# Kernel tuning notes

Hardware: AMD Instinct MI355X
Metric: run time of the kernel (lower is better)

The kernel has to match this reference:

```python
import jax, jax.numpy as jnp
import numpy as np

B, T, S, C, E, H = 4, 2048, 2048, 256, 512, 8
D = E // H
SCALE = E ** (-0.5)


def setup_inputs() -> dict:
    key = jax.random.key(0)
    ks = jax.random.split(key, 12)
    x = jax.random.normal(ks[0], (B, T, C), dtype=jnp.float32)
    context = jax.random.normal(ks[1], (B, S, E), dtype=jnp.float32)
    pad_mask = jax.random.randint(ks[2], (B, T, S), 0, 2) == 1
    p = 0.02
    # Conv1d kernel_size=1 weights stored squeezed: [out_ch, in_ch]
    w_in = jax.random.normal(ks[3], (E, C), dtype=jnp.float32) * p
    b_in = jnp.zeros((E,), dtype=jnp.float32)
    wq = jax.random.normal(ks[4], (E, E), dtype=jnp.float32) * p
    bq = jnp.zeros((E,), dtype=jnp.float32)
    wk = jax.random.normal(ks[5], (E, E), dtype=jnp.float32) * p
    bk = jnp.zeros((E,), dtype=jnp.float32)
    wv = jax.random.normal(ks[6], (E, E), dtype=jnp.float32) * p
    bv = jnp.zeros((E,), dtype=jnp.float32)
    w_out = jax.random.normal(ks[7], (C, E), dtype=jnp.float32) * p
    b_out = jnp.zeros((C,), dtype=jnp.float32)
    return {"x": x, "context": context, "pad_mask": pad_mask,
            "w_in": w_in, "b_in": b_in, "wq": wq, "bq": bq,
            "wk": wk, "bk": bk, "wv": wv, "bv": bv,
            "w_out": w_out, "b_out": b_out}


def reference(x, context, pad_mask, w_in, b_in, wq, bq, wk, bk, wv, bv, w_out, b_out):
    # proj_in: Conv1d k=1 == per-token linear on channel dim. [B,T,C] -> [B,T,E]
    xe = jnp.einsum('btc,ec->bte', x, w_in) + b_in
    Q = (xe @ wq.T + bq).reshape(B, T, H, D)       # query tokens
    K = (context @ wk.T + bk).reshape(B, S, H, D)  # key tokens
    V = (context @ wv.T + bv).reshape(B, S, H, D)
    att = jnp.einsum('bihd,bjhd->bhij', Q, K) * SCALE  # [B,H,T,S]
    att = jnp.where(pad_mask[:, None, :, :], jnp.float32(-1e9), att)
    att = jax.nn.softmax(att, axis=-1)
    out = jnp.einsum('bhij,bjhd->bihd', att, V).reshape(B, T, E)
    # proj_out: Conv1d k=1, [B,T,E] -> [B,T,C]
    out = jnp.einsum('bte,ce->btc', out, w_out) + b_out
    return out
```

## Files before the change

### kernel.cpp

```cpp
#include <hip/hip_runtime.h>
#include <cstdint>
#include <cstddef>

#define Bb 4
#define Tt 2048
#define Ssz 2048
#define Cc 256
#define Ee 512
#define Hh 8

typedef short bf8 __attribute__((ext_vector_type(8)));
typedef float f4 __attribute__((ext_vector_type(4)));

__device__ __forceinline__ unsigned short f2bf(float x) {
  unsigned int u = __float_as_uint(x);
  u += 0x7fffu + ((u >> 16) & 1u);
  return (unsigned short)(u >> 16);
}

__device__ __forceinline__ bf8 cvt8(float4 a, float4 b) {
  bf8 r;
  r[0] = (short)f2bf(a.x); r[1] = (short)f2bf(a.y);
  r[2] = (short)f2bf(a.z); r[3] = (short)f2bf(a.w);
  r[4] = (short)f2bf(b.x); r[5] = (short)f2bf(b.y);
  r[6] = (short)f2bf(b.z); r[7] = (short)f2bf(b.w);
  return r;
}

__global__ __launch_bounds__(256) void prep(const float* __restrict__ w_in,
                                            const float* __restrict__ b_in,
                                            const float* __restrict__ wq,
                                            const float* __restrict__ bq,
                                            const float* __restrict__ wk,
                                            const float* __restrict__ wv,
                                            const float* __restrict__ wo,
                                            unsigned short* __restrict__ wkvb,
                                            unsigned short* __restrict__ wob,
                                            unsigned short* __restrict__ wqin,
                                            float* __restrict__ bqinb, float qsc) {
  __shared__ unsigned short sh[128][72];
  const int bid = blockIdx.x, tid = threadIdx.x;
  if (bid < 512) {
    int i = bid * 256 + tid;
    const float* s = (i < 65536) ? wk : wv;
    int off = (i < 65536) ? i : i - 65536;
    float4 v = ((const float4*)s)[off];
    ushort4 o;
    o.x = f2bf(v.x); o.y = f2bf(v.y); o.z = f2bf(v.z); o.w = f2bf(v.w);
    ((ushort4*)wkvb)[i] = o;
  } else if (bid < 640) {
    int i = (bid - 512) * 256 + tid;
    float4 v = ((const float4*)wo)[i];
    ushort4 o;
    o.x = f2bf(v.x); o.y = f2bf(v.y); o.z = f2bf(v.z); o.w = f2bf(v.w);
    ((ushort4*)wob)[i] = o;
  } else if (bid < 672) {
    const int idx = bid - 640;
    const int m0 = (idx & 7) * 64, n0 = (idx >> 3) * 64;
    unsigned short (*As)[72] = (unsigned short (*)[72]) & sh[0][0];
    unsigned short (*Bs)[72] = (unsigned short (*)[72]) & sh[64][0];
    const int wave = tid >> 6, lane = tid & 63;
    const int lrow = lane & 15, quad = lane >> 4;
    const int wm = (wave >> 1) * 32, wn = (wave & 1) * 32;
    const int arow = tid >> 3, ac = tid & 7;
    f4 acc[2][2];
#pragma unroll
    for (int i = 0; i < 2; i++)
#pragma unroll
      for (int j = 0; j < 2; j++) {
        f4 z = {0.f, 0.f, 0.f, 0.f};
        acc[i][j] = z;
      }
    for (int kt = 0; kt < 8; kt++) {
#pragma unroll
      for (int i = 0; i < 2; i++) {
        int row = arow + i * 32;
        const float* src = wq + (size_t)(m0 + row) * Ee + kt * 64 + ac * 8;
        float4 v0 = *(const float4*)src, v1 = *(const float4*)(src + 4);
        bf8 av;
        av[0] = (short)f2bf(v0.x * qsc); av[1] = (short)f2bf(v0.y * qsc);
        av[2] = (short)f2bf(v0.z * qsc); av[3] = (short)f2bf(v0.w * qsc);
        av[4] = (short)f2bf(v1.x * qsc); av[5] = (short)f2bf(v1.y * qsc);
        av[6] = (short)f2bf(v1.z * qsc); av[7] = (short)f2bf(v1.w * qsc);
        *(bf8*)&As[row][ac * 8] = av;
        int c = n0 + row;
        bf8 bv;
#pragma unroll
        for (int k = 0; k < 8; k++)
          bv[k] = (short)f2bf(w_in[(size_t)(kt * 64 + ac * 8 + k) * Cc + c]);
        *(bf8*)&Bs[row][ac * 8] = bv;
      }
      __syncthreads();
#pragma unroll
      for (int kk = 0; kk < 2; kk++) {
        bf8 af[2], bff[2];
#pragma unroll
        for (int i = 0; i < 2; i++) af[i] = *(const bf8*)&As[wm + i * 16 + lrow][kk * 32 + quad * 8];
#pragma unroll
        for (int j = 0; j < 2; j++) bff[j] = *(const bf8*)&Bs[wn + j * 16 + lrow][kk * 32 + quad * 8];
#pragma unroll
        for (int i = 0; i < 2; i++)
#pragma unroll
          for (int j = 0; j < 2; j++)
            acc[i][j] = __builtin_amdgcn_mfma_f32_16x16x32_bf16(af[i], bff[j], acc[i][j], 0, 0, 0);
      }
      __syncthreads();
    }
#pragma unroll
    for (int j = 0; j < 2; j++)
#pragma unroll
      for (int i = 0; i < 2; i++)
#pragma unroll
        for (int r = 0; r < 4; r++)
          wqin[(size_t)(m0 + wm + i * 16 + quad * 4 + r) * Cc + n0 + wn + j * 16 + lrow] =
              f2bf(acc[i][j][r]);
  } else {
    const int o = (bid - 672) * 32 + (tid >> 3);
    const int k0 = (tid & 7) * 64;
    float s = 0.f;
#pragma unroll
    for (int i = 0; i < 16; i++) {
      float4 w = *(const float4*)(wq + (size_t)o * Ee + k0 + i * 4);
      float4 bb = *(const float4*)(b_in + k0 + i * 4);
      s += w.x * bb.x + w.y * bb.y + w.z * bb.z + w.w * bb.w;
    }
    s += __shfl_xor(s, 1);
    s += __shfl_xor(s, 2);
    s += __shfl_xor(s, 4);
    if ((tid & 7) == 0) bqinb[o] = (s + bq[o]) * qsc;
  }
}

__global__ __launch_bounds__(256) void qkv(const float* __restrict__ x,
                                           const float* __restrict__ ctx,
                                           const unsigned short* __restrict__ wqin,
                                           const float* __restrict__ bqinb,
                                           const unsigned short* __restrict__ wkv,
                                           const float* __restrict__ bk,
                                           const float* __restrict__ bv,
                                           unsigned short* __restrict__ Qb,
                                           unsigned short* __restrict__ Kb,
                                           unsigned short* __restrict__ Vt,
                                           const int* __restrict__ mask,
                                           unsigned int* __restrict__ mp) {
  __shared__ unsigned short As[128][72];
  __shared__ unsigned short Bs[128][72];
  const int bid = blockIdx.x, tid = threadIdx.x;
  if (bid >= 768) {
    int i = (bid - 768) * 256 + tid;
    const int4* src = (const int4*)mask + (size_t)i * 8;
    unsigned int w = 0;
#pragma unroll
    for (int k = 0; k < 8; k++) {
      int4 v = src[k];
      w |= (unsigned int)(v.x != 0) << (k * 4);
      w |= (unsigned int)(v.y != 0) << (k * 4 + 1);
      w |= (unsigned int)(v.z != 0) << (k * 4 + 2);
      w |= (unsigned int)(v.w != 0) << (k * 4 + 3);
    }
    mp[i] = w;
    return;
  }
  const bool isQ = bid < 256;
  const int idx = isQ ? bid : bid - 256;
  const int m0 = (idx & 63) * 128;
  const int n0 = (idx >> 6) * 128;
  const int K = isQ ? 256 : 512;
  const float* A = isQ ? x : ctx;
  const unsigned short* Bt = isQ ? wqin : wkv;

  const int wave = tid >> 6, lane = tid & 63;
  const int lrow = lane & 15, quad = lane >> 4;
  const int wm = (wave >> 1) * 64, wn = (wave & 1) * 64;
  const int arow = tid >> 3, ac = tid & 7;

  f4 acc[4][4];
#pragma unroll
  for (int i = 0; i < 4; i++)
#pragma unroll
    for (int j = 0; j < 4; j++) {
      f4 z = {0.f, 0.f, 0.f, 0.f};
      acc[i][j] = z;
    }

  float4 ap0[4], ap1[4];
  bf8 bpre[4];
#pragma unroll
  for (int i = 0; i < 4; i++) {
    const float* src = A + (size_t)(m0 + arow + i * 32) * K + ac * 8;
    ap0[i] = *(const float4*)src;
    ap1[i] = *(const float4*)(src + 4);
    bpre[i] = *(const bf8*)(Bt + (size_t)(n0 + arow + i * 32) * K + ac * 8);
  }

  const int nkt = K >> 6;
  for (int kt = 0; kt < nkt; ++kt) {
#pragma unroll
    for (int i = 0; i < 4; i++) {
      *(bf8*)&As[arow + i * 32][ac * 8] = cvt8(ap0[i], ap1[i]);
      *(bf8*)&Bs[arow + i * 32][ac * 8] = bpre[i];
    }
    __syncthreads();
    if (kt + 1 < nkt) {
      int k0 = (kt + 1) << 6;
#pragma unroll
      for (int i = 0; i < 4; i++) {
        const float* src = A + (size_t)(m0 + arow + i * 32) * K + k0 + ac * 8;
        ap0[i] = *(const float4*)src;
        ap1[i] = *(const float4*)(src + 4);
        bpre[i] = *(const bf8*)(Bt + (size_t)(n0 + arow + i * 32) * K + k0 + ac * 8);
      }
    }
#pragma unroll
    for (int kk = 0; kk < 2; kk++) {
      bf8 af[4], bff[4];
#pragma unroll
      for (int i = 0; i < 4; i++)
        af[i] = *(const bf8*)&As[wm + i * 16 + lrow][kk * 32 + quad * 8];
#pragma unroll
      for (int j = 0; j < 4; j++)
        bff[j] = *(const bf8*)&Bs[wn + j * 16 + lrow][kk * 32 + quad * 8];
#pragma unroll
      for (int i = 0; i < 4; i++)
#pragma unroll
        for (int j = 0; j < 4; j++)
          acc[i][j] = __builtin_amdgcn_mfma_f32_16x16x32_bf16(af[i], bff[j],
                                                              acc[i][j], 0, 0, 0);
    }
    __syncthreads();
  }

  if (isQ) {
#pragma unroll
    for (int j = 0; j < 4; j++) {
      int col = n0 + wn + j * 16 + lrow;
      float bvv = bqinb[col];
#pragma unroll
      for (int i = 0; i < 4; i++)
#pragma unroll
        for (int r = 0; r < 4; r++)
          Qb[(size_t)(m0 + wm + i * 16 + quad * 4 + r) * Ee + col] =
              f2bf(acc[i][j][r] + bvv);
    }
  } else if (n0 < 512) {
#pragma unroll
    for (int j = 0; j < 4; j++) {
      int col = n0 + wn + j * 16 + lrow;
      float bvv = bk[col];
#pragma unroll
      for (int i = 0; i < 4; i++)
#pragma unroll
        for (int r = 0; r < 4; r++)
          Kb[(size_t)(m0 + wm + i * 16 + quad * 4 + r) * Ee + col] =
              f2bf(acc[i][j][r] + bvv);
    }
  } else {
#pragma unroll
    for (int j = 0; j < 4; j++) {
      int d = n0 - 512 + wn + j * 16 + lrow;
      int h = d >> 6, dd = d & 63;
      float bvv = bv[d];
#pragma unroll
      for (int i = 0; i < 4; i++) {
        int tok = m0 + wm + i * 16 + quad * 4;
        int b = tok >> 11, sl = tok & 2047;
        ushort4 pk;
        pk.x = f2bf(acc[i][j][0] + bvv);
        pk.y = f2bf(acc[i][j][1] + bvv);
        pk.z = f2bf(acc[i][j][2] + bvv);
        pk.w = f2bf(acc[i][j][3] + bvv);
        *(ushort4*)(Vt + (size_t)((b * Hh + h) * 64 + dd) * Ssz + sl) = pk;
      }
    }
  }
}

template <bool OUT_BF16, int BM, int BN, int WGM>
__global__ __launch_bounds__(256) void gemm_bt(const unsigned short* __restrict__ A,
                                               const unsigned short* __restrict__ Bt,
                                               const float* __restrict__ bias0,
                                               void* __restrict__ Cout,
                                               int M, int N, int K) {
  constexpr int WGN = 4 / WGM;
  constexpr int MI = BM / (WGM * 16);
  constexpr int NJ = BN / (WGN * 16);
  constexpr int NA = BM / 32;
  constexpr int NB = BN / 32;
  __shared__ unsigned short As[BM][72];
  __shared__ unsigned short Bs[BN][72];
  const int tid = threadIdx.x;
  const int wave = tid >> 6, lane = tid & 63;
  const int lrow = lane & 15, quad = lane >> 4;
  const int wm = (wave / WGN) * (BM / WGM);
  const int wn = (wave % WGN) * (BN / WGN);
  const int m0 = blockIdx.x * BM, n0 = blockIdx.y * BN;
  const int arow = tid >> 3, ac = tid & 7;

  f4 acc[MI][NJ];
#pragma unroll
  for (int i = 0; i < MI; i++)
#pragma unroll
    for (int j = 0; j < NJ; j++) {
      f4 z = {0.f, 0.f, 0.f, 0.f};
      acc[i][j] = z;
    }

  bf8 apre[NA], bpre[NB];
#pragma unroll
  for (int i = 0; i < NA; i++)
    apre[i] = *(const bf8*)(A + (size_t)(m0 + arow + i * 32) * K + ac * 8);
#pragma unroll
  for (int i = 0; i < NB; i++)
    bpre[i] = *(const bf8*)(Bt + (size_t)(n0 + arow + i * 32) * K + ac * 8);

  const int nkt = K >> 6;
  for (int kt = 0; kt < nkt; ++kt) {
#pragma unroll
    for (int i = 0; i < NA; i++) *(bf8*)&As[arow + i * 32][ac * 8] = apre[i];
#pragma unroll
    for (int i = 0; i < NB; i++) *(bf8*)&Bs[arow + i * 32][ac * 8] = bpre[i];
    __syncthreads();
    if (kt + 1 < nkt) {
      int k0 = (kt + 1) << 6;
#pragma unroll
      for (int i = 0; i < NA; i++)
        apre[i] = *(const bf8*)(A + (size_t)(m0 + arow + i * 32) * K + k0 + ac * 8);
#pragma unroll
      for (int i = 0; i < NB; i++)
        bpre[i] = *(const bf8*)(Bt + (size_t)(n0 + arow + i * 32) * K + k0 + ac * 8);
    }
#pragma unroll
    for (int kk = 0; kk < 2; kk++) {
      bf8 af[MI], bff[NJ];
#pragma unroll
      for (int i = 0; i < MI; i++)
        af[i] = *(const bf8*)&As[wm + i * 16 + lrow][kk * 32 + quad * 8];
#pragma unroll
      for (int j = 0; j < NJ; j++)
        bff[j] = *(const bf8*)&Bs[wn + j * 16 + lrow][kk * 32 + quad * 8];
#pragma unroll
      for (int i = 0; i < MI; i++)
#pragma unroll
        for (int j = 0; j < NJ; j++)
          acc[i][j] = __builtin_amdgcn_mfma_f32_16x16x32_bf16(af[i], bff[j],
                                                              acc[i][j], 0, 0, 0);
    }
    __syncthreads();
  }

#pragma unroll
  for (int j = 0; j < NJ; j++) {
    int col = n0 + wn + j * 16 + lrow;
    float bvv = bias0 ? bias0[col] : 0.f;
#pragma unroll
    for (int i = 0; i < MI; i++) {
#pragma unroll
      for (int r = 0; r < 4; r++) {
        int row = m0 + wm + i * 16 + quad * 4 + r;
        float v = acc[i][j][r] + bvv;
        if (OUT_BF16)
          ((unsigned short*)Cout)[(size_t)row * N + col] = f2bf(v);
        else
          ((float*)Cout)[(size_t)row * N + col] = v;
      }
    }
  }
}

__global__ __launch_bounds__(256) void attn(const unsigned short* __restrict__ Q,
                                            const unsigned short* __restrict__ K,
                                            const unsigned short* __restrict__ Vt,
                                            const unsigned int* __restrict__ mp,
                                            unsigned short* __restrict__ O) {
  __shared__ unsigned short Ks[64][72];
  __shared__ unsigned short Vts[64][72];
  __shared__ unsigned short Ps[128][72];
  const int tid = threadIdx.x;
  const int wave = tid >> 6, lane = tid & 63;
  const int lrow = lane & 15, quad = lane >> 4;
  const int bid = blockIdx.x;
  const int bh = bid & 31, b = bh >> 3, h = bh & 7;
  const int t0 = (bid >> 5) * 128;
  const int arow = tid >> 3, ac = tid & 7;
  const int wm = wave * 32;

#pragma unroll
  for (int i = 0; i < 4; i++) {
    int row = arow + i * 32;
    *(bf8*)&Ps[row][ac * 8] =
        *(const bf8*)(Q + (size_t)(b * Tt + t0 + row) * Ee + h * 64 + ac * 8);
  }
  __syncthreads();
  bf8 qf[2][2];
#pragma unroll
  for (int mi = 0; mi < 2; mi++) {
    qf[mi][0] = *(const bf8*)&Ps[wm + mi * 16 + lrow][quad * 8];
    qf[mi][1] = *(const bf8*)&Ps[wm + mi * 16 + lrow][32 + quad * 8];
  }

  f4 oacc[2][4];
  f4 dacc[2];
#pragma unroll
  for (int mi = 0; mi < 2; mi++) {
    f4 z = {0.f, 0.f, 0.f, 0.f};
    dacc[mi] = z;
#pragma unroll
    for (int j = 0; j < 4; j++) oacc[mi][j] = z;
  }
  bf8 ones;
#pragma unroll
  for (int k = 0; k < 8; k++) ones[k] = (short)0x3F80;

  const unsigned short* Kbase = K + (size_t)b * Ssz * Ee + h * 64;
  const unsigned short* Vbase = Vt + (size_t)((b * Hh + h) * 64) * Ssz;
  const unsigned int* mrow0 = mp + (size_t)(b * Tt + t0 + wm + lrow) * 64;
  const unsigned int* mrow1 = mp + (size_t)(b * Tt + t0 + wm + 16 + lrow) * 64;

  bf8 kreg[2], vreg[2];
#pragma unroll
  for (int i = 0; i < 2; i++) {
    int row = arow + i * 32;
    kreg[i] = *(const bf8*)(Kbase + (size_t)row * Ee + ac * 8);
    vreg[i] = *(const bf8*)(Vbase + (size_t)row * Ssz + ac * 8);
  }

  for (int s0 = 0; s0 < Ssz; s0 += 64) {
    __syncthreads();
#pragma unroll
    for (int i = 0; i < 2; i++) {
      int row = arow + i * 32;
      *(bf8*)&Ks[row][ac * 8] = kreg[i];
      *(bf8*)&Vts[row][ac * 8] = vreg[i];
    }
    __syncthreads();
    if (s0 + 64 < Ssz) {
#pragma unroll
      for (int i = 0; i < 2; i++) {
        int row = arow + i * 32;
        kreg[i] = *(const bf8*)(Kbase + (size_t)(s0 + 64 + row) * Ee + ac * 8);
        vreg[i] = *(const bf8*)(Vbase + (size_t)row * Ssz + s0 + 64 + ac * 8);
      }
    }
    const uint2 mw0 = *(const uint2*)(mrow0 + (s0 >> 5));
    const uint2 mw1 = *(const uint2*)(mrow1 + (s0 >> 5));

#pragma unroll
    for (int sf = 0; sf < 4; sf++) {
      bf8 kf0 = *(const bf8*)&Ks[sf * 16 + lrow][quad * 8];
      bf8 kf1 = *(const bf8*)&Ks[sf * 16 + lrow][32 + quad * 8];
      f4 sa[2];
      f4 z = {0.f, 0.f, 0.f, 0.f};
      sa[0] = z; sa[1] = z;
      sa[0] = __builtin_amdgcn_mfma_f32_16x16x32_bf16(kf0, qf[0][0], sa[0], 0, 0, 0);
      sa[0] = __builtin_amdgcn_mfma_f32_16x16x32_bf16(kf1, qf[0][1], sa[0], 0, 0, 0);
      sa[1] = __builtin_amdgcn_mfma_f32_16x16x32_bf16(kf0, qf[1][0], sa[1], 0, 0, 0);
      sa[1] = __builtin_amdgcn_mfma_f32_16x16x32_bf16(kf1, qf[1][1], sa[1], 0, 0, 0);
#pragma unroll
      for (int mi = 0; mi < 2; mi++) {
        const uint2 mw = mi ? mw1 : mw0;
        const unsigned int w = (sf >= 2) ? mw.y : mw.x;
        ushort4 pk;
#pragma unroll
        for (int r = 0; r < 4; r++) {
          const unsigned int bit = (sf & 1) * 16 + quad * 4 + r;
          float e = __builtin_amdgcn_exp2f(sa[mi][r]);
          float p = ((w >> bit) & 1u) ? 0.f : e;
          unsigned short pb = (unsigned short)(__float_as_uint(p) >> 16);
          if (r == 0) pk.x = pb;
          else if (r == 1) pk.y = pb;
          else if (r == 2) pk.z = pb;
          else pk.w = pb;
        }
        *(ushort4*)&Ps[wm + mi * 16 + lrow][sf * 16 + quad * 4] = pk;
      }
    }
#pragma unroll
    for (int kk = 0; kk < 2; kk++) {
      bf8 pf[2];
#pragma unroll
      for (int mi = 0; mi < 2; mi++) {
        pf[mi] = *(const bf8*)&Ps[wm + mi * 16 + lrow][kk * 32 + quad * 8];
        dacc[mi] = __builtin_amdgcn_mfma_f32_16x16x32_bf16(pf[mi], ones, dacc[mi], 0, 0, 0);
      }
#pragma unroll
      for (int j = 0; j < 4; j++) {
        bf8 vf = *(const bf8*)&Vts[j * 16 + lrow][kk * 32 + quad * 8];
#pragma unroll
        for (int mi = 0; mi < 2; mi++)
          oacc[mi][j] = __builtin_amdgcn_mfma_f32_16x16x32_bf16(pf[mi], vf, oacc[mi][j], 0, 0, 0);
      }
    }
  }

#pragma unroll
  for (int mi = 0; mi < 2; mi++) {
#pragma unroll
    for (int r = 0; r < 4; r++) {
      float inv = 1.0f / dacc[mi][r];
      int row = b * Tt + t0 + wm + mi * 16 + quad * 4 + r;
#pragma unroll
      for (int j = 0; j < 4; j++)
        O[(size_t)row * Ee + h * 64 + j * 16 + lrow] = f2bf(oacc[mi][j][r] * inv);
    }
  }
}

extern "C" void kernel_launch(void* const* d_in, const int* in_sizes, int n_in,
                              void* d_out, int out_size, void* d_ws, size_t ws_size,
                              hipStream_t stream) {
  const float* x    = (const float*)d_in[0];
  const float* ctx  = (const float*)d_in[1];
  const int*   mask = (const int*)d_in[2];
  const float* w_in = (const float*)d_in[3];
  const float* b_in = (const float*)d_in[4];
  const float* wq   = (const float*)d_in[5];
  const float* bq   = (const float*)d_in[6];
  const float* wk   = (const float*)d_in[7];
  const float* bk   = (const float*)d_in[8];
  const float* wv   = (const float*)d_in[9];
  const float* bv   = (const float*)d_in[10];
  const float* wo   = (const float*)d_in[11];
  const float* bo   = (const float*)d_in[12];

  const float qsc = 0.04419417382415922f * 1.4426950408889634f;

  unsigned short* ws = (unsigned short*)d_ws;
  unsigned int*   maskp = (unsigned int*)ws;
  unsigned short* wkvb  = ws + 1048576;
  unsigned short* wob   = ws + 1572864;
  unsigned short* wqin  = ws + 1703936;
  float*          bqinb = (float*)(ws + 1835008);
  unsigned short* Qb    = ws + 1836032;
  unsigned short* Kb    = ws + 6030336;
  unsigned short* Vtb   = ws + 10224640;
  unsigned short* Ob    = ws + 14418944;

  prep<<<688, 256, 0, stream>>>(w_in, b_in, wq, bq, wk, wv, wo,
                                wkvb, wob, wqin, bqinb, qsc);
  qkv<<<2816, 256, 0, stream>>>(x, ctx, wqin, bqinb, wkvb, bk, bv, Qb, Kb, Vtb,
                                mask, maskp);
  attn<<<512, 256, 0, stream>>>(Qb, Kb, Vtb, maskp, Ob);
  gemm_bt<false, 64, 64, 2><<<dim3(128, 4), 256, 0, stream>>>(
      Ob, wob, bo, d_out, 8192, 256, 512);
}
```

Baseline: 237.6 us.

## Load K/V fragments directly from global into registers, drop LDS staging

The attention kernel no longer stages K and V tiles through shared memory with two block barriers per step. Each lane now loads its MFMA fragments straight from global memory, K double-buffered in registers one tile ahead and V loaded at the start of each step. The P pack uses a byte-permute instruction and the kernel declares launch bounds for two blocks per CU. This removes LDS traffic and syncs, but each wave fetches K/V redundantly from global/L2 with less coalesced accesses and higher register pressure. A barrier remains, and the P buffer in LDS is still shared per wave.

```diff
diff --git a/kernel.cpp b/kernel.cpp
--- a/kernel.cpp
+++ b/kernel.cpp
@@ -26,6 +26,12 @@
   r[6] = (short)f2bf(b.z); r[7] = (short)f2bf(b.w);
   return r;
 }
+
+#if __has_builtin(__builtin_amdgcn_perm)
+#define PACK2(u0, u1) __builtin_amdgcn_perm((u1), (u0), 0x07060302u)
+#else
+#define PACK2(u0, u1) (((u0) >> 16) | ((u1) & 0xffff0000u))
+#endif
 
 __global__ __launch_bounds__(256) void prep(const float* __restrict__ w_in,
                                             const float* __restrict__ b_in,
@@ -367,13 +373,11 @@
   }
 }
 
-__global__ __launch_bounds__(256) void attn(const unsigned short* __restrict__ Q,
-                                            const unsigned short* __restrict__ K,
-                                            const unsigned short* __restrict__ Vt,
-                                            const unsigned int* __restrict__ mp,
-                                            unsigned short* __restrict__ O) {
-  __shared__ unsigned short Ks[64][72];
-  __shared__ unsigned short Vts[64][72];
+__global__ __launch_bounds__(256, 2) void attn(const unsigned short* __restrict__ Q,
+                                               const unsigned short* __restrict__ K,
+                                               const unsigned short* __restrict__ Vt,
+                                               const unsigned int* __restrict__ mp,
+                                               unsigned short* __restrict__ O) {
   __shared__ unsigned short Ps[128][72];
   const int tid = threadIdx.x;
   const int wave = tid >> 6, lane = tid & 63;
@@ -381,22 +385,16 @@
   const int bid = blockIdx.x;
   const int bh = bid & 31, b = bh >> 3, h = bh & 7;
   const int t0 = (bid >> 5) * 128;
-  const int arow = tid >> 3, ac = tid & 7;
   const int wm = wave * 32;
 
-#pragma unroll
-  for (int i = 0; i < 4; i++) {
-    int row = arow + i * 32;
-    *(bf8*)&Ps[row][ac * 8] =
-        *(const bf8*)(Q + (size_t)(b * Tt + t0 + row) * Ee + h * 64 + ac * 8);
-  }
-  __syncthreads();
+  const unsigned short* Ql =
+      Q + (size_t)(b * Tt + t0 + wm + lrow) * Ee + h * 64 + quad * 8;
   bf8 qf[2][2];
 #pragma unroll
-  for (int mi = 0; mi < 2; mi++) {
-    qf[mi][0] = *(const bf8*)&Ps[wm + mi * 16 + lrow][quad * 8];
-    qf[mi][1] = *(const bf8*)&Ps[wm + mi * 16 + lrow][32 + quad * 8];
-  }
+  for (int mi = 0; mi < 2; mi++)
+#pragma unroll
+    for (int kk = 0; kk < 2; kk++)
+      qf[mi][kk] = *(const bf8*)(Ql + (size_t)(mi * 16) * Ee + kk * 32);
 
   f4 oacc[2][4];
   f4 dacc[2];
@@ -411,69 +409,62 @@
 #pragma unroll
   for (int k = 0; k < 8; k++) ones[k] = (short)0x3F80;
 
-  const unsigned short* Kbase = K + (size_t)b * Ssz * Ee + h * 64;
-  const unsigned short* Vbase = Vt + (size_t)((b * Hh + h) * 64) * Ssz;
+  const unsigned short* Kl =
+      K + (size_t)(b * Ssz + lrow) * Ee + h * 64 + quad * 8;
+  const unsigned short* Vl =
+      Vt + (size_t)((b * Hh + h) * 64 + lrow) * Ssz + quad * 8;
   const unsigned int* mrow0 = mp + (size_t)(b * Tt + t0 + wm + lrow) * 64;
   const unsigned int* mrow1 = mp + (size_t)(b * Tt + t0 + wm + 16 + lrow) * 64;
 
-  bf8 kreg[2], vreg[2];
-#pragma unroll
-  for (int i = 0; i < 2; i++) {
-    int row = arow + i * 32;
-    kreg[i] = *(const bf8*)(Kbase + (size_t)row * Ee + ac * 8);
-    vreg[i] = *(const bf8*)(Vbase + (size_t)row * Ssz + ac * 8);
-  }
-
-  for (int s0 = 0; s0 < Ssz; s0 += 64) {
-    __syncthreads();
-#pragma unroll
-    for (int i = 0; i < 2; i++) {
-      int row = arow + i * 32;
-      *(bf8*)&Ks[row][ac * 8] = kreg[i];
-      *(bf8*)&Vts[row][ac * 8] = vreg[i];
-    }
-    __syncthreads();
-    if (s0 + 64 < Ssz) {
-#pragma unroll
-      for (int i = 0; i < 2; i++) {
-        int row = arow + i * 32;
-        kreg[i] = *(const bf8*)(Kbase + (size_t)(s0 + 64 + row) * Ee + ac * 8);
-        vreg[i] = *(const bf8*)(Vbase + (size_t)row * Ssz + s0 + 64 + ac * 8);
-      }
-    }
+  bf8 ka[4][2], kb[4][2];
+
+  auto pfk = [&](bf8 (&KD)[4][2], int s0) {
+#pragma unroll
+    for (int sf = 0; sf < 4; sf++)
+#pragma unroll
+      for (int kk = 0; kk < 2; kk++)
+        KD[sf][kk] = *(const bf8*)(Kl + (size_t)(s0 + sf * 16) * Ee + kk * 32);
+  };
+
+  auto body = [&](bf8 (&KF)[4][2], bf8 (&KN)[4][2], int s0, bool dopf) {
+    __builtin_amdgcn_s_barrier();
+    bf8 vf[4][2];
+#pragma unroll
+    for (int j = 0; j < 4; j++)
+#pragma unroll
+      for (int kk = 0; kk < 2; kk++)
+        vf[j][kk] = *(const bf8*)(Vl + (size_t)(j * 16) * Ssz + s0 + kk * 32);
     const uint2 mw0 = *(const uint2*)(mrow0 + (s0 >> 5));
     const uint2 mw1 = *(const uint2*)(mrow1 + (s0 >> 5));
 
 #pragma unroll
     for (int sf = 0; sf < 4; sf++) {
-      bf8 kf0 = *(const bf8*)&Ks[sf * 16 + lrow][quad * 8];
-      bf8 kf1 = *(const bf8*)&Ks[sf * 16 + lrow][32 + quad * 8];
-      f4 sa[2];
       f4 z = {0.f, 0.f, 0.f, 0.f};
-      sa[0] = z; sa[1] = z;
-      sa[0] = __builtin_amdgcn_mfma_f32_16x16x32_bf16(kf0, qf[0][0], sa[0], 0, 0, 0);
-      sa[0] = __builtin_amdgcn_mfma_f32_16x16x32_bf16(kf1, qf[0][1], sa[0], 0, 0, 0);
-      sa[1] = __builtin_amdgcn_mfma_f32_16x16x32_bf16(kf0, qf[1][0], sa[1], 0, 0, 0);
-      sa[1] = __builtin_amdgcn_mfma_f32_16x16x32_bf16(kf1, qf[1][1], sa[1], 0, 0, 0);
+      f4 sa0 = z, sa1 = z;
+      sa0 = __builtin_amdgcn_mfma_f32_16x16x32_bf16(KF[sf][0], qf[0][0], sa0, 0, 0, 0);
+      sa0 = __builtin_amdgcn_mfma_f32_16x16x32_bf16(KF[sf][1], qf[0][1], sa0, 0, 0, 0);
+      sa1 = __builtin_amdgcn_mfma_f32_16x16x32_bf16(KF[sf][0], qf[1][0], sa1, 0, 0, 0);
+      sa1 = __builtin_amdgcn_mfma_f32_16x16x32_bf16(KF[sf][1], qf[1][1], sa1, 0, 0, 0);
 #pragma unroll
       for (int mi = 0; mi < 2; mi++) {
+        const f4 sa = mi ? sa1 : sa0;
         const uint2 mw = mi ? mw1 : mw0;
         const unsigned int w = (sf >= 2) ? mw.y : mw.x;
-        ushort4 pk;
+        const unsigned int nib = w >> ((sf & 1) * 16 + quad * 4);
+        unsigned int u[4];
 #pragma unroll
         for (int r = 0; r < 4; r++) {
-          const unsigned int bit = (sf & 1) * 16 + quad * 4 + r;
-          float e = __builtin_amdgcn_exp2f(sa[mi][r]);
-          float p = ((w >> bit) & 1u) ? 0.f : e;
-          unsigned short pb = (unsigned short)(__float_as_uint(p) >> 16);
-          if (r == 0) pk.x = pb;
-          else if (r == 1) pk.y = pb;
-          else if (r == 2) pk.z = pb;
-          else pk.w = pb;
+          float e = __builtin_amdgcn_exp2f(sa[r]);
+          float p = ((nib >> r) & 1u) ? 0.f : e;
+          u[r] = __float_as_uint(p);
         }
-        *(ushort4*)&Ps[wm + mi * 16 + lrow][sf * 16 + quad * 4] = pk;
-      }
-    }
+        uint2 pw;
+        pw.x = PACK2(u[0], u[1]);
+        pw.y = PACK2(u[2], u[3]);
+        *(uint2*)&Ps[wm + mi * 16 + lrow][sf * 16 + quad * 4] = pw;
+      }
+    }
+    if (dopf) pfk(KN, s0 + 64);
 #pragma unroll
     for (int kk = 0; kk < 2; kk++) {
       bf8 pf[2];
@@ -483,13 +474,18 @@
         dacc[mi] = __builtin_amdgcn_mfma_f32_16x16x32_bf16(pf[mi], ones, dacc[mi], 0, 0, 0);
       }
 #pragma unroll
-      for (int j = 0; j < 4; j++) {
-        bf8 vf = *(const bf8*)&Vts[j * 16 + lrow][kk * 32 + quad * 8];
+      for (int j = 0; j < 4; j++)
 #pragma unroll
         for (int mi = 0; mi < 2; mi++)
-          oacc[mi][j] = __builtin_amdgcn_mfma_f32_16x16x32_bf16(pf[mi], vf, oacc[mi][j], 0, 0, 0);
-      }
-    }
+          oacc[mi][j] = __builtin_amdgcn_mfma_f32_16x16x32_bf16(pf[mi], vf[j][kk],
+                                                               oacc[mi][j], 0, 0, 0);
+    }
+  };
+
+  pfk(ka, 0);
+  for (int s0 = 0; s0 < Ssz; s0 += 128) {
+    body(ka, kb, s0, true);
+    body(kb, ka, s0 + 64, s0 + 128 < Ssz);
   }
 
 #pragma unroll
```

After: 300.8 us. 26.6% more time.

## Rewrite attention with 32x32 MFMA, register-resident P, and double-buffered K/V

Applied to the files above, without the earlier changes.

The attention kernel moves from 16x16x32 to 32x32x16 bf16 MFMA tiles. The probability tile now stays in registers: it is packed with perm and laid out for the PV MFMA with permlane32 swaps, so the LDS round trip for P is gone. The pad mask is folded into the score accumulator's initial value (-1e9) rather than selected after the exp. K/V tiles are double-buffered in LDS so there is one barrier per iteration instead of two. It also sets launch bounds for two blocks per CU, which risks register pressure with three 16-wide accumulators.

```diff
diff --git a/kernel.cpp b/kernel.cpp
--- a/kernel.cpp
+++ b/kernel.cpp
@@ -11,6 +11,9 @@
 
 typedef short bf8 __attribute__((ext_vector_type(8)));
 typedef float f4 __attribute__((ext_vector_type(4)));
+typedef float f16v __attribute__((ext_vector_type(16)));
+typedef unsigned int u32x2 __attribute__((ext_vector_type(2)));
+typedef unsigned int u32x4 __attribute__((ext_vector_type(4)));
 
 __device__ __forceinline__ unsigned short f2bf(float x) {
   unsigned int u = __float_as_uint(x);
@@ -25,6 +28,31 @@
   r[4] = (short)f2bf(b.x); r[5] = (short)f2bf(b.y);
   r[6] = (short)f2bf(b.z); r[7] = (short)f2bf(b.w);
   return r;
+}
+
+#if __has_builtin(__builtin_amdgcn_perm)
+#define PACK2(u0, u1) __builtin_amdgcn_perm((u1), (u0), 0x07060302u)
+#else
+#define PACK2(u0, u1) (((u0) >> 16) | ((u1) & 0xffff0000u))
+#endif
+
+#define EXPU(v) __float_as_uint(__builtin_amdgcn_exp2f(v))
+#define MFMA32(a, b, c) __builtin_amdgcn_mfma_f32_32x32x16_bf16((a), (b), (c), 0, 0, 0)
+
+__device__ __forceinline__ void pl32swap(unsigned int& a, unsigned int& b) {
+#if __has_builtin(__builtin_amdgcn_permlane32_swap)
+  u32x2 r = __builtin_amdgcn_permlane32_swap(a, b, false, false);
+  a = r[0];
+  b = r[1];
+#else
+  unsigned int ax = (unsigned int)__shfl_xor((int)a, 32);
+  unsigned int bx = (unsigned int)__shfl_xor((int)b, 32);
+  bool hi = (threadIdx.x & 32) != 0;
+  unsigned int an = hi ? bx : a;
+  unsigned int bn = hi ? b : ax;
+  a = an;
+  b = bn;
+#endif
 }
 
 __global__ __launch_bounds__(256) void prep(const float* __restrict__ w_in,
@@ -367,45 +395,34 @@
   }
 }
 
-__global__ __launch_bounds__(256) void attn(const unsigned short* __restrict__ Q,
-                                            const unsigned short* __restrict__ K,
-                                            const unsigned short* __restrict__ Vt,
-                                            const unsigned int* __restrict__ mp,
-                                            unsigned short* __restrict__ O) {
-  __shared__ unsigned short Ks[64][72];
-  __shared__ unsigned short Vts[64][72];
-  __shared__ unsigned short Ps[128][72];
+__global__ __launch_bounds__(256, 2) void attn(const unsigned short* __restrict__ Q,
+                                               const unsigned short* __restrict__ K,
+                                               const unsigned short* __restrict__ Vt,
+                                               const unsigned int* __restrict__ mp,
+                                               unsigned short* __restrict__ O) {
+  __shared__ unsigned short Ks[2][64][72];
+  __shared__ unsigned short Vts[2][64][72];
   const int tid = threadIdx.x;
   const int wave = tid >> 6, lane = tid & 63;
-  const int lrow = lane & 15, quad = lane >> 4;
+  const int l31 = lane & 31, hi = lane >> 5;
   const int bid = blockIdx.x;
   const int bh = bid & 31, b = bh >> 3, h = bh & 7;
   const int t0 = (bid >> 5) * 128;
+  const int wm = wave * 32;
   const int arow = tid >> 3, ac = tid & 7;
-  const int wm = wave * 32;
-
-#pragma unroll
-  for (int i = 0; i < 4; i++) {
-    int row = arow + i * 32;
-    *(bf8*)&Ps[row][ac * 8] =
-        *(const bf8*)(Q + (size_t)(b * Tt + t0 + row) * Ee + h * 64 + ac * 8);
-  }
-  __syncthreads();
-  bf8 qf[2][2];
-#pragma unroll
-  for (int mi = 0; mi < 2; mi++) {
-    qf[mi][0] = *(const bf8*)&Ps[wm + mi * 16 + lrow][quad * 8];
-    qf[mi][1] = *(const bf8*)&Ps[wm + mi * 16 + lrow][32 + quad * 8];
-  }
-
-  f4 oacc[2][4];
-  f4 dacc[2];
-#pragma unroll
-  for (int mi = 0; mi < 2; mi++) {
-    f4 z = {0.f, 0.f, 0.f, 0.f};
-    dacc[mi] = z;
-#pragma unroll
-    for (int j = 0; j < 4; j++) oacc[mi][j] = z;
+
+  const unsigned short* Qrow =
+      Q + (size_t)(b * Tt + t0 + wm + l31) * Ee + h * 64 + hi * 8;
+  bf8 qf[4];
+#pragma unroll
+  for (int c = 0; c < 4; c++) qf[c] = *(const bf8*)(Qrow + c * 16);
+
+  f16v oacc0, oacc1, dacc;
+#pragma unroll
+  for (int r = 0; r < 16; r++) {
+    oacc0[r] = 0.f;
+    oacc1[r] = 0.f;
+    dacc[r] = 0.f;
   }
   bf8 ones;
 #pragma unroll
@@ -413,8 +430,7 @@
 
   const unsigned short* Kbase = K + (size_t)b * Ssz * Ee + h * 64;
   const unsigned short* Vbase = Vt + (size_t)((b * Hh + h) * 64) * Ssz;
-  const unsigned int* mrow0 = mp + (size_t)(b * Tt + t0 + wm + lrow) * 64;
-  const unsigned int* mrow1 = mp + (size_t)(b * Tt + t0 + wm + 16 + lrow) * 64;
+  const unsigned int* mroww = mp + (size_t)(b * Tt + t0 + wm + l31) * 64;
 
   bf8 kreg[2], vreg[2];
 #pragma unroll
@@ -423,17 +439,18 @@
     kreg[i] = *(const bf8*)(Kbase + (size_t)row * Ee + ac * 8);
     vreg[i] = *(const bf8*)(Vbase + (size_t)row * Ssz + ac * 8);
   }
-
-  for (int s0 = 0; s0 < Ssz; s0 += 64) {
-    __syncthreads();
-#pragma unroll
-    for (int i = 0; i < 2; i++) {
-      int row = arow + i * 32;
-      *(bf8*)&Ks[row][ac * 8] = kreg[i];
-      *(bf8*)&Vts[row][ac * 8] = vreg[i];
-    }
-    __syncthreads();
-    if (s0 + 64 < Ssz) {
+#pragma unroll
+  for (int i = 0; i < 2; i++) {
+    int row = arow + i * 32;
+    *(bf8*)&Ks[0][row][ac * 8] = kreg[i];
+    *(bf8*)&Vts[0][row][ac * 8] = vreg[i];
+  }
+  __syncthreads();
+
+  for (int n = 0; n < 32; n++) {
+    const int s0 = n * 64;
+    const int cur = n & 1;
+    if (n + 1 < 32) {
 #pragma unroll
       for (int i = 0; i < 2; i++) {
         int row = arow + i * 32;
@@ -441,67 +458,68 @@
         vreg[i] = *(const bf8*)(Vbase + (size_t)row * Ssz + s0 + 64 + ac * 8);
       }
     }
-    const uint2 mw0 = *(const uint2*)(mrow0 + (s0 >> 5));
-    const uint2 mw1 = *(const uint2*)(mrow1 + (s0 >> 5));
-
-#pragma unroll
-    for (int sf = 0; sf < 4; sf++) {
-      bf8 kf0 = *(const bf8*)&Ks[sf * 16 + lrow][quad * 8];
-      bf8 kf1 = *(const bf8*)&Ks[sf * 16 + lrow][32 + quad * 8];
-      f4 sa[2];
-      f4 z = {0.f, 0.f, 0.f, 0.f};
-      sa[0] = z; sa[1] = z;
-      sa[0] = __builtin_amdgcn_mfma_f32_16x16x32_bf16(kf0, qf[0][0], sa[0], 0, 0, 0);
-      sa[0] = __builtin_amdgcn_mfma_f32_16x16x32_bf16(kf1, qf[0][1], sa[0], 0, 0, 0);
-      sa[1] = __builtin_amdgcn_mfma_f32_16x16x32_bf16(kf0, qf[1][0], sa[1], 0, 0, 0);
-      sa[1] = __builtin_amdgcn_mfma_f32_16x16x32_bf16(kf1, qf[1][1], sa[1], 0, 0, 0);
-#pragma unroll
-      for (int mi = 0; mi < 2; mi++) {
-        const uint2 mw = mi ? mw1 : mw0;
-        const unsigned int w = (sf >= 2) ? mw.y : mw.x;
-        ushort4 pk;
-#pragma unroll
-        for (int r = 0; r < 4; r++) {
-          const unsigned int bit = (sf & 1) * 16 + quad * 4 + r;
-          float e = __builtin_amdgcn_exp2f(sa[mi][r]);
-          float p = ((w >> bit) & 1u) ? 0.f : e;
-          unsigned short pb = (unsigned short)(__float_as_uint(p) >> 16);
-          if (r == 0) pk.x = pb;
-          else if (r == 1) pk.y = pb;
-          else if (r == 2) pk.z = pb;
-          else pk.w = pb;
-        }
-        *(ushort4*)&Ps[wm + mi * 16 + lrow][sf * 16 + quad * 4] = pk;
-      }
-    }
-#pragma unroll
-    for (int kk = 0; kk < 2; kk++) {
-      bf8 pf[2];
-#pragma unroll
-      for (int mi = 0; mi < 2; mi++) {
-        pf[mi] = *(const bf8*)&Ps[wm + mi * 16 + lrow][kk * 32 + quad * 8];
-        dacc[mi] = __builtin_amdgcn_mfma_f32_16x16x32_bf16(pf[mi], ones, dacc[mi], 0, 0, 0);
-      }
-#pragma unroll
-      for (int j = 0; j < 4; j++) {
-        bf8 vf = *(const bf8*)&Vts[j * 16 + lrow][kk * 32 + quad * 8];
-#pragma unroll
-        for (int mi = 0; mi < 2; mi++)
-          oacc[mi][j] = __builtin_amdgcn_mfma_f32_16x16x32_bf16(pf[mi], vf, oacc[mi][j], 0, 0, 0);
-      }
-    }
-  }
-
-#pragma unroll
-  for (int mi = 0; mi < 2; mi++) {
-#pragma unroll
-    for (int r = 0; r < 4; r++) {
-      float inv = 1.0f / dacc[mi][r];
-      int row = b * Tt + t0 + wm + mi * 16 + quad * 4 + r;
-#pragma unroll
-      for (int j = 0; j < 4; j++)
-        O[(size_t)row * Ee + h * 64 + j * 16 + lrow] = f2bf(oacc[mi][j][r] * inv);
-    }
+    const uint2 mw = *(const uint2*)(mroww + (s0 >> 5));
+    const unsigned int wsh0 = mw.x >> (4 * hi);
+    const unsigned int wsh1 = mw.y >> (4 * hi);
+
+    f16v sa0, sa1;
+#pragma unroll
+    for (int r = 0; r < 16; r++) {
+      const int sh = (r & 3) + 8 * (r >> 2);
+      sa0[r] = ((wsh0 >> sh) & 1u) ? -1e9f : 0.f;
+      sa1[r] = ((wsh1 >> sh) & 1u) ? -1e9f : 0.f;
+    }
+#pragma unroll
+    for (int c = 0; c < 4; c++) {
+      bf8 kf0 = *(const bf8*)&Ks[cur][l31][c * 16 + hi * 8];
+      bf8 kf1 = *(const bf8*)&Ks[cur][32 + l31][c * 16 + hi * 8];
+      sa0 = MFMA32(kf0, qf[c], sa0);
+      sa1 = MFMA32(kf1, qf[c], sa1);
+    }
+    unsigned int X0[8], X1[8];
+#pragma unroll
+    for (int m = 0; m < 8; m++) {
+      X0[m] = PACK2(EXPU(sa0[2 * m]), EXPU(sa0[2 * m + 1]));
+      X1[m] = PACK2(EXPU(sa1[2 * m]), EXPU(sa1[2 * m + 1]));
+    }
+#pragma unroll
+    for (int c = 0; c < 4; c++) {
+      const int m0 = 4 * (c & 1);
+      unsigned int a0, a1, a2, a3;
+      if (c < 2) {
+        a0 = X0[m0]; a1 = X0[m0 + 1]; a2 = X0[m0 + 2]; a3 = X0[m0 + 3];
+      } else {
+        a0 = X1[m0]; a1 = X1[m0 + 1]; a2 = X1[m0 + 2]; a3 = X1[m0 + 3];
+      }
+      pl32swap(a0, a2);
+      pl32swap(a1, a3);
+      u32x4 pdv;
+      pdv[0] = a0; pdv[1] = a1; pdv[2] = a2; pdv[3] = a3;
+      bf8 pa = *(bf8*)&pdv;
+      bf8 vf0 = *(const bf8*)&Vts[cur][l31][c * 16 + hi * 8];
+      bf8 vf1 = *(const bf8*)&Vts[cur][32 + l31][c * 16 + hi * 8];
+      dacc = MFMA32(pa, ones, dacc);
+      oacc0 = MFMA32(pa, vf0, oacc0);
+      oacc1 = MFMA32(pa, vf1, oacc1);
+    }
+    if (n + 1 < 32) {
+#pragma unroll
+      for (int i = 0; i < 2; i++) {
+        int row = arow + i * 32;
+        *(bf8*)&Ks[cur ^ 1][row][ac * 8] = kreg[i];
+        *(bf8*)&Vts[cur ^ 1][row][ac * 8] = vreg[i];
+      }
+    }
+    __syncthreads();
+  }
+
+#pragma unroll
+  for (int r = 0; r < 16; r++) {
+    const int tl = (r & 3) + 8 * (r >> 2) + 4 * hi;
+    const float inv = 1.0f / dacc[r];
+    const size_t off = (size_t)(b * Tt + t0 + wm + tl) * Ee + h * 64 + l31;
+    O[off] = f2bf(oacc0[r] * inv);
+    O[off + 32] = f2bf(oacc1[r] * inv);
   }
 }
 
```

New measurement: 228.3 us. 1.04x faster.
